# Kernel optimization log

Measured on AMD Instinct MI355X. Metric: run time of the kernel, lower is better.

The kernel has to match this reference:

```python
import jax, jax.numpy as jnp
import numpy as np

ALPHA = 0.2  # LeakyReLU negative slope


def setup_inputs() -> dict:
    key = jax.random.key(0)
    k1, k2, k3, k4 = jax.random.split(key, 4)
    B, N, Fin, H, Fout = 4, 2048, 128, 4, 32
    x = jax.random.normal(k1, (B, N, Fin), dtype=jnp.float32)
    adj = jax.random.randint(k2, (B, N, N), 0, 2, dtype=jnp.int32)
    # xavier-ish scaled params
    W = jax.random.normal(k3, (Fin, Fout * H), dtype=jnp.float32) * (2.0 / (Fin + Fout * H)) ** 0.5
    att = jax.random.normal(k4, (1, H, 2 * Fout), dtype=jnp.float32) * (2.0 / (1 + 2 * Fout)) ** 0.5
    self_weight = jnp.ones((1,), dtype=jnp.float32)
    return {"x": x, "adj": adj, "W": W, "att": att, "self_weight": self_weight}


def reference(x, adj, W, att, self_weight):
    B, N, _ = x.shape
    H = att.shape[1]
    Fh = att.shape[2] // 2
    # h: [B, N, H, Fh]
    h = (x @ W).reshape(B, N, H, Fh)
    a = att[0]  # [H, 2*Fh]
    # cat(h_i, h_j) . att == e_i[b,n,h] + e_j[b,m,h]  (no O(N^2 F) materialization)
    e_i = jnp.einsum('bnhf,hf->bnh', h, a[:, :Fh])
    e_j = jnp.einsum('bmhf,hf->bmh', h, a[:, Fh:])
    scores = e_i[:, :, None, :] + e_j[:, None, :, :]  # [B, N, N, H]
    scores = jnp.where(scores > 0, scores, ALPHA * scores)  # LeakyReLU
    scores = jnp.where(adj[..., None] == 0, -jnp.inf, scores)
    attn = jax.nn.softmax(scores, axis=2)  # softmax over m (neighbors)
    # faithful to einsum('bnmh,bnhf->bnhf'): contract attn over m, scale h at node n
    messages = attn.sum(axis=2)[..., None] * h
    out = messages + h * self_weight  # self_weight broadcasts (shape [1])
    return out.reshape(B, N, H * Fh)
```

## Files before the change

### kernel.cpp

```cpp
#include <hip/hip_runtime.h>


typedef __attribute__((ext_vector_type(8))) short short8;
typedef __attribute__((ext_vector_type(4))) float f32x4;

__device__ __forceinline__ unsigned short f32_to_bf16(float f) {
    unsigned int u = __builtin_bit_cast(unsigned int, f);
    u += 0x7fffu + ((u >> 16) & 1u);
    return (unsigned short)(u >> 16);
}

__device__ __forceinline__ short8 load8_f32_as_bf16(const float* __restrict__ p) {
    f32x4 lo = *(const f32x4*)p;
    f32x4 hi = *(const f32x4*)(p + 4);
    short8 r;
    r[0] = (short)f32_to_bf16(lo[0]); r[1] = (short)f32_to_bf16(lo[1]);
    r[2] = (short)f32_to_bf16(lo[2]); r[3] = (short)f32_to_bf16(lo[3]);
    r[4] = (short)f32_to_bf16(hi[0]); r[5] = (short)f32_to_bf16(hi[1]);
    r[6] = (short)f32_to_bf16(hi[2]); r[7] = (short)f32_to_bf16(hi[3]);
    return r;
}

#define KDIM 128
#define NDIM 128
#define LDS_STRIDE 136

__global__ __launch_bounds__(256) void gat_as_gemm(
    const float* __restrict__ x,
    const float* __restrict__ W,
    const float* __restrict__ swp,
    float* __restrict__ out)
{
    __shared__ unsigned short WT[NDIM * LDS_STRIDE];

    const int tid = threadIdx.x;

    #pragma unroll
    for (int it = 0; it < 8; ++it) {
        int c  = it * 256 + tid;
        int k  = c & 127;
        int nb = (c >> 7) << 3;
        const float* src = W + k * NDIM + nb;
        f32x4 lo = *(const f32x4*)src;
        f32x4 hi = *(const f32x4*)(src + 4);
        #pragma unroll
        for (int j = 0; j < 4; ++j) {
            WT[(nb + j) * LDS_STRIDE + k]     = f32_to_bf16(lo[j]);
            WT[(nb + 4 + j) * LDS_STRIDE + k] = f32_to_bf16(hi[j]);
        }
    }

    const float scale = 1.0f + swp[0];

    __syncthreads();

    const int wave = tid >> 6;
    const int lane = tid & 63;
    const int q = lane >> 4;
    const int r = lane & 15;
    const int m0 = blockIdx.x * 64 + wave * 16;

    const float* xrow = x + (size_t)(m0 + r) * KDIM + q * 8;
    short8 a0 = load8_f32_as_bf16(xrow + 0);
    short8 a1 = load8_f32_as_bf16(xrow + 32);
    short8 a2 = load8_f32_as_bf16(xrow + 64);
    short8 a3 = load8_f32_as_bf16(xrow + 96);

    #pragma unroll
    for (int nt = 0; nt < 8; ++nt) {
        const unsigned short* wrow = &WT[(nt * 16 + r) * LDS_STRIDE + q * 8];
        short8 b0 = *(const short8*)(wrow + 0);
        short8 b1 = *(const short8*)(wrow + 32);
        short8 b2 = *(const short8*)(wrow + 64);
        short8 b3 = *(const short8*)(wrow + 96);

        f32x4 acc = {0.f, 0.f, 0.f, 0.f};
        acc = __builtin_amdgcn_mfma_f32_16x16x32_bf16(a0, b0, acc, 0, 0, 0);
        acc = __builtin_amdgcn_mfma_f32_16x16x32_bf16(a1, b1, acc, 0, 0, 0);
        acc = __builtin_amdgcn_mfma_f32_16x16x32_bf16(a2, b2, acc, 0, 0, 0);
        acc = __builtin_amdgcn_mfma_f32_16x16x32_bf16(a3, b3, acc, 0, 0, 0);

        const int col = nt * 16 + r;
        #pragma unroll
        for (int reg = 0; reg < 4; ++reg) {
            int row = m0 + q * 4 + reg;
            out[(size_t)row * NDIM + col] = scale * acc[reg];
        }
    }
}

extern "C" void kernel_launch(void* const* d_in, const int* in_sizes, int n_in,
                              void* d_out, int out_size, void* d_ws, size_t ws_size,
                              hipStream_t stream) {
    const float* x  = (const float*)d_in[0];
    const float* W  = (const float*)d_in[2];
    const float* sw = (const float*)d_in[4];
    float* out = (float*)d_out;

    const int M = in_sizes[0] / KDIM;
    const int grid = M / 64;

    gat_as_gemm<<<grid, 256, 0, stream>>>(x, W, sw, out);
}
```

Measured before the change: 99.54 us.

## Split output columns across two blocks and vectorize stores via transposed MFMA

```diff
diff --git a/kernel.cpp b/kernel.cpp
--- a/kernel.cpp
+++ b/kernel.cpp
@@ -31,22 +31,25 @@
     const float* __restrict__ swp,
     float* __restrict__ out)
 {
-    __shared__ unsigned short WT[NDIM * LDS_STRIDE];
+    __shared__ unsigned short WT[64 * LDS_STRIDE];
 
     const int tid = threadIdx.x;
+    const int bx  = blockIdx.x;
+    const int rb  = bx >> 1;
+    const int c0  = (bx & 1) * 64;
 
     #pragma unroll
-    for (int it = 0; it < 8; ++it) {
+    for (int it = 0; it < 4; ++it) {
         int c  = it * 256 + tid;
         int k  = c & 127;
-        int nb = (c >> 7) << 3;
-        const float* src = W + k * NDIM + nb;
+        int nl = (c >> 7) << 3;
+        const float* src = W + k * NDIM + c0 + nl;
         f32x4 lo = *(const f32x4*)src;
         f32x4 hi = *(const f32x4*)(src + 4);
         #pragma unroll
         for (int j = 0; j < 4; ++j) {
-            WT[(nb + j) * LDS_STRIDE + k]     = f32_to_bf16(lo[j]);
-            WT[(nb + 4 + j) * LDS_STRIDE + k] = f32_to_bf16(hi[j]);
+            WT[(nl + j) * LDS_STRIDE + k]     = f32_to_bf16(lo[j]);
+            WT[(nl + 4 + j) * LDS_STRIDE + k] = f32_to_bf16(hi[j]);
         }
     }
 
@@ -58,34 +61,30 @@
     const int lane = tid & 63;
     const int q = lane >> 4;
     const int r = lane & 15;
-    const int m0 = blockIdx.x * 64 + wave * 16;
+    const int m0 = rb * 64 + wave * 16;
 
     const float* xrow = x + (size_t)(m0 + r) * KDIM + q * 8;
-    short8 a0 = load8_f32_as_bf16(xrow + 0);
-    short8 a1 = load8_f32_as_bf16(xrow + 32);
-    short8 a2 = load8_f32_as_bf16(xrow + 64);
-    short8 a3 = load8_f32_as_bf16(xrow + 96);
+    short8 x0 = load8_f32_as_bf16(xrow + 0);
+    short8 x1 = load8_f32_as_bf16(xrow + 32);
+    short8 x2 = load8_f32_as_bf16(xrow + 64);
+    short8 x3 = load8_f32_as_bf16(xrow + 96);
 
     #pragma unroll
-    for (int nt = 0; nt < 8; ++nt) {
+    for (int nt = 0; nt < 4; ++nt) {
         const unsigned short* wrow = &WT[(nt * 16 + r) * LDS_STRIDE + q * 8];
-        short8 b0 = *(const short8*)(wrow + 0);
-        short8 b1 = *(const short8*)(wrow + 32);
-        short8 b2 = *(const short8*)(wrow + 64);
-        short8 b3 = *(const short8*)(wrow + 96);
+        short8 w0 = *(const short8*)(wrow + 0);
+        short8 w1 = *(const short8*)(wrow + 32);
+        short8 w2 = *(const short8*)(wrow + 64);
+        short8 w3 = *(const short8*)(wrow + 96);
 
         f32x4 acc = {0.f, 0.f, 0.f, 0.f};
-        acc = __builtin_amdgcn_mfma_f32_16x16x32_bf16(a0, b0, acc, 0, 0, 0);
-        acc = __builtin_amdgcn_mfma_f32_16x16x32_bf16(a1, b1, acc, 0, 0, 0);
-        acc = __builtin_amdgcn_mfma_f32_16x16x32_bf16(a2, b2, acc, 0, 0, 0);
-        acc = __builtin_amdgcn_mfma_f32_16x16x32_bf16(a3, b3, acc, 0, 0, 0);
+        acc = __builtin_amdgcn_mfma_f32_16x16x32_bf16(w0, x0, acc, 0, 0, 0);
+        acc = __builtin_amdgcn_mfma_f32_16x16x32_bf16(w1, x1, acc, 0, 0, 0);
+        acc = __builtin_amdgcn_mfma_f32_16x16x32_bf16(w2, x2, acc, 0, 0, 0);
+        acc = __builtin_amdgcn_mfma_f32_16x16x32_bf16(w3, x3, acc, 0, 0, 0);
 
-        const int col = nt * 16 + r;
-        #pragma unroll
-        for (int reg = 0; reg < 4; ++reg) {
-            int row = m0 + q * 4 + reg;
-            out[(size_t)row * NDIM + col] = scale * acc[reg];
-        }
+        f32x4 v = {scale * acc[0], scale * acc[1], scale * acc[2], scale * acc[3]};
+        *(f32x4*)(out + (size_t)(m0 + r) * NDIM + c0 + nt * 16 + q * 4) = v;
     }
 }
 
@@ -98,7 +97,7 @@
     float* out = (float*)d_out;
 
     const int M = in_sizes[0] / KDIM;
-    const int grid = M / 64;
+    const int grid = (M / 64) * 2;
 
     gat_as_gemm<<<grid, 256, 0, stream>>>(x, W, sw, out);
 }
```

New measurement: 98.67 us. About the same (-0.9%).
